# Kernel tuning notes

Measured on AMD Instinct MI355X. Metric: run time of the kernel, lower is better.

The kernel has to match this reference:

```python
import jax, jax.numpy as jnp
import numpy as np

N = 100000      # nodes
E = 3200000     # edges (avg degree 32)
F_IN = 128      # num_node_features
H = 16          # hidden dim (fixed in module)
C = 2           # num_classes


def setup_inputs() -> dict:
    key = jax.random.key(0)
    k0, k1, k2, k3 = jax.random.split(key, 4)
    x = jax.random.normal(k0, (N, F_IN), dtype=jnp.float32)
    edge_index = jax.random.randint(k1, (2, E), 0, N, dtype=jnp.int32)
    # GCNConv params: weight (in,out) + bias (out,) per layer (glorot-ish scale)
    W1 = jax.random.normal(k2, (F_IN, H), dtype=jnp.float32) * (1.0 / np.sqrt(F_IN))
    b1 = jnp.zeros((H,), jnp.float32)
    W2 = jax.random.normal(k3, (H, C), dtype=jnp.float32) * (1.0 / np.sqrt(H))
    b2 = jnp.zeros((C,), jnp.float32)
    return {"x": x, "edge_index": edge_index, "W1": W1, "b1": b1, "W2": W2, "b2": b2}


def _gcn_conv(x, W, b, src, dst, n):
    # GCNConv: h = D^{-1/2}(A+I)D^{-1/2} (x W) + b, with self-loops in src/dst
    h = x @ W                                   # [n, out]
    deg = jax.ops.segment_sum(jnp.ones_like(dst, dtype=h.dtype), dst, num_segments=n)
    dinv = jnp.where(deg > 0, jax.lax.rsqrt(deg), 0.0)
    norm = dinv[src] * dinv[dst]                # [E+n]
    msg = h[src] * norm[:, None]                # gather + scale
    out = jax.ops.segment_sum(msg, dst, num_segments=n)  # scatter-add
    return out + b


def reference(x, edge_index, W1, b1, W2, b2):
    loops = jnp.arange(N, dtype=edge_index.dtype)
    src = jnp.concatenate([edge_index[0], loops])
    dst = jnp.concatenate([edge_index[1], loops])
    h = jax.nn.relu(_gcn_conv(x, W1, b1, src, dst, N))
    # F.dropout(training=False) in eval mode is identity
    out = _gcn_conv(h, W2, b2, src, dst, N)
    return jax.nn.log_softmax(out, axis=1)
```

## Files before the change

kernel.cpp:

```cpp
#include <hip/hip_runtime.h>
#include <hip/hip_bf16.h>

#define NN 100000
#define NE 3200000
#define FIN 128
#define HD 16
#define CD 2

#define BSH 8
#define BSPAN 256
#define NBKT 391
#define CHUNK 8192
#define NPB ((NE + CHUNK - 1) / CHUNK)

__device__ __forceinline__ float bf2f(ushort u) {
    union { float f; unsigned int i; } v; v.i = ((unsigned int)u) << 16; return v.f;
}
__device__ __forceinline__ ushort f2b(float f) {
    union { float f; unsigned int u; } v; v.f = f;
    unsigned int r = (v.u + 0x7FFFu + ((v.u >> 16) & 1u)) >> 16;
    return (ushort)r;
}

__global__ __launch_bounds__(512) void k_cnt(const int* __restrict__ dst,
                                             int* __restrict__ cntmat) {
    __shared__ int h[NBKT];
    for (int i = threadIdx.x; i < NBKT; i += 512) h[i] = 0;
    __syncthreads();
    int cq = blockIdx.x * (CHUNK / 4);
    const int4* d4 = (const int4*)dst;
    #pragma unroll
    for (int j = 0; j < CHUNK / 2048; ++j) {
        int e4 = cq + j * 512 + threadIdx.x;
        if (e4 < NE / 4) {
            int4 d = d4[e4];
            atomicAdd(&h[d.x >> BSH], 1);
            atomicAdd(&h[d.y >> BSH], 1);
            atomicAdd(&h[d.z >> BSH], 1);
            atomicAdd(&h[d.w >> BSH], 1);
        }
    }
    __syncthreads();
    int* row = cntmat + (size_t)blockIdx.x * NBKT;
    for (int i = threadIdx.x; i < NBKT; i += 512) row[i] = h[i];
}

__global__ __launch_bounds__(256) void k_colscan(const int* __restrict__ cntmat,
                                                 int* __restrict__ relm,
                                                 int* __restrict__ btot) {
    __shared__ int sm[256];
    int j = blockIdx.x, t = threadIdx.x;
    int v[2];
    int b0 = t * 2;
    #pragma unroll
    for (int k = 0; k < 2; ++k) {
        int b = b0 + k;
        v[k] = (b < NPB) ? cntmat[(size_t)b * NBKT + j] : 0;
    }
    sm[t] = v[0] + v[1];
    __syncthreads();
    for (int off = 1; off < 256; off <<= 1) {
        int x = 0;
        if (t >= off) x = sm[t - off];
        __syncthreads();
        if (t >= off) sm[t] += x;
        __syncthreads();
    }
    int run = (t == 0) ? 0 : sm[t - 1];
    int* rrow = relm + (size_t)j * NPB;
    #pragma unroll
    for (int k = 0; k < 2; ++k) {
        int b = b0 + k;
        if (b < NPB) rrow[b] = run;
        run += v[k];
    }
    if (t == 255) btot[j] = sm[255];
}

__global__ __launch_bounds__(512) void k_scanb(const int* __restrict__ btot,
                                               int* __restrict__ boff) {
    __shared__ int sm[512];
    int t = threadIdx.x;
    sm[t] = (t < NBKT) ? btot[t] : 0;
    __syncthreads();
    for (int off = 1; off < 512; off <<= 1) {
        int v = 0;
        if (t >= off) v = sm[t - off];
        __syncthreads();
        if (t >= off) sm[t] += v;
        __syncthreads();
    }
    if (t < NBKT) boff[t] = t ? sm[t - 1] : 0;
    if (t == 511) boff[NBKT] = sm[511];
}

__global__ __launch_bounds__(512) void k_part(const int* __restrict__ src,
                                              const int* __restrict__ dst,
                                              const int* __restrict__ boff,
                                              const int* __restrict__ relm,
                                              unsigned int* __restrict__ csrb) {
    __shared__ int cur[NBKT];
    int b = blockIdx.x, t = threadIdx.x;
    for (int i = t; i < NBKT; i += 512)
        cur[i] = boff[i] + relm[(size_t)i * NPB + b];
    __syncthreads();
    int cq = b * (CHUNK / 4);
    const int4* s4 = (const int4*)src;
    const int4* d4 = (const int4*)dst;
    #pragma unroll
    for (int j = 0; j < CHUNK / 2048; ++j) {
        int e4 = cq + j * 512 + t;
        if (e4 < NE / 4) {
            int4 s = s4[e4];
            int4 d = d4[e4];
            int p;
            p = atomicAdd(&cur[d.x >> BSH], 1);
            csrb[p] = (unsigned)s.x | ((unsigned)(d.x & (BSPAN - 1)) << 17);
            p = atomicAdd(&cur[d.y >> BSH], 1);
            csrb[p] = (unsigned)s.y | ((unsigned)(d.y & (BSPAN - 1)) << 17);
            p = atomicAdd(&cur[d.z >> BSH], 1);
            csrb[p] = (unsigned)s.z | ((unsigned)(d.z & (BSPAN - 1)) << 17);
            p = atomicAdd(&cur[d.w >> BSH], 1);
            csrb[p] = (unsigned)s.w | ((unsigned)(d.w & (BSPAN - 1)) << 17);
        }
    }
}

__global__ __launch_bounds__(512) void k_sortb(const int* __restrict__ boff,
                                               const unsigned int* __restrict__ csrb,
                                               int* __restrict__ csr2,
                                               int* __restrict__ rowptr,
                                               float* __restrict__ dinv) {
    __shared__ int cnt[BSPAN];
    __shared__ int sc[BSPAN];
    __shared__ int cur[BSPAN];
    int b = blockIdx.x, t = threadIdx.x;
    if (t < BSPAN) cnt[t] = 0;
    __syncthreads();
    int e0 = boff[b], e1 = boff[b + 1];
    for (int e = e0 + t; e < e1; e += 512) atomicAdd(&cnt[csrb[e] >> 17], 1);
    __syncthreads();
    if (t < BSPAN) sc[t] = cnt[t];
    __syncthreads();
    for (int off = 1; off < BSPAN; off <<= 1) {
        int v = 0;
        if (t < BSPAN && t >= off) v = sc[t - off];
        __syncthreads();
        if (t < BSPAN && t >= off) sc[t] += v;
        __syncthreads();
    }
    if (t < BSPAN) {
        int ex = e0 + (t ? sc[t - 1] : 0);
        cur[t] = ex;
        int node = b * BSPAN + t;
        if (node < NN) {
            rowptr[node] = ex;
            dinv[node] = rsqrtf((float)cnt[t] + 1.0f);
        }
    }
    if (b == 0 && t == 0) rowptr[NN] = boff[NBKT];
    __syncthreads();
    for (int e = e0 + t; e < e1; e += 512) {
        unsigned p = csrb[e];
        int pos = atomicAdd(&cur[p >> 17], 1);
        csr2[pos] = (int)(p & 0x1FFFF);
    }
}

__global__ __launch_bounds__(256) void k_gemm1(const float* __restrict__ x,
                                               const float* __restrict__ W1,
                                               const float* __restrict__ dinv,
                                               ushort* __restrict__ h1b) {
    __shared__ float wsm[FIN][HD];
    for (int i = threadIdx.x; i < FIN * HD; i += 256) wsm[i >> 4][i & 15] = W1[i];
    __syncthreads();
    int t = blockIdx.x * 256 + threadIdx.x;
    int node = t >> 2;
    if (node >= NN) return;
    int g = (t & 3) * 4;
    const float4* xr = (const float4*)(x + (size_t)node * FIN);
    float a0 = 0.f, a1 = 0.f, a2 = 0.f, a3 = 0.f;
    #pragma unroll
    for (int k4 = 0; k4 < FIN / 4; ++k4) {
        float4 v = xr[k4];
        #pragma unroll
        for (int kk = 0; kk < 4; ++kk) {
            float vk = (kk == 0) ? v.x : (kk == 1) ? v.y : (kk == 2) ? v.z : v.w;
            float4 w = *(const float4*)&wsm[k4 * 4 + kk][g];
            a0 += vk * w.x;
            a1 += vk * w.y;
            a2 += vk * w.z;
            a3 += vk * w.w;
        }
    }
    float di = dinv[node];
    ushort4 r = {f2b(a0 * di), f2b(a1 * di), f2b(a2 * di), f2b(a3 * di)};
    *(ushort4*)(h1b + (size_t)node * HD + g) = r;
}

__global__ __launch_bounds__(256) void k_agg1(const int* __restrict__ rowptr,
                                              const int* __restrict__ csr2,
                                              const ushort* __restrict__ h1b,
                                              const float* __restrict__ dinv,
                                              const float* __restrict__ b1,
                                              const float* __restrict__ W2,
                                              float* __restrict__ g_s) {
    int wid = (blockIdx.x * 256 + threadIdx.x) >> 6;
    int lane = threadIdx.x & 63;
    int node = wid * 4 + (lane >> 4);
    if (node >= NN) return;
    int l16 = lane & 15;
    int slot = l16 >> 2;
    int fq = (lane & 3) * 4;
    int e0 = rowptr[node], e1 = rowptr[node + 1];
    float a0 = 0.f, a1 = 0.f, a2 = 0.f, a3 = 0.f;
    float c0 = 0.f, c1 = 0.f, c2 = 0.f, c3 = 0.f;
    int e = e0 + slot;
    for (; e + 4 < e1; e += 8) {
        int s0 = csr2[e];
        int s1 = csr2[e + 4];
        ushort4 u0 = *(const ushort4*)(h1b + (size_t)s0 * HD + fq);
        ushort4 u1 = *(const ushort4*)(h1b + (size_t)s1 * HD + fq);
        a0 += bf2f(u0.x); a1 += bf2f(u0.y); a2 += bf2f(u0.z); a3 += bf2f(u0.w);
        c0 += bf2f(u1.x); c1 += bf2f(u1.y); c2 += bf2f(u1.z); c3 += bf2f(u1.w);
    }
    if (e < e1) {
        ushort4 u = *(const ushort4*)(h1b + (size_t)csr2[e] * HD + fq);
        a0 += bf2f(u.x); a1 += bf2f(u.y); a2 += bf2f(u.z); a3 += bf2f(u.w);
    }
    a0 += c0; a1 += c1; a2 += c2; a3 += c3;
    #pragma unroll
    for (int m = 4; m <= 8; m <<= 1) {
        a0 += __shfl_xor(a0, m, 64);
        a1 += __shfl_xor(a1, m, 64);
        a2 += __shfl_xor(a2, m, 64);
        a3 += __shfl_xor(a3, m, 64);
    }
    if (slot == 0) {
        float di = dinv[node];
        ushort4 us = *(const ushort4*)(h1b + (size_t)node * HD + fq);
        float v0 = fmaxf(di * (a0 + bf2f(us.x)) + b1[fq],     0.f);
        float v1 = fmaxf(di * (a1 + bf2f(us.y)) + b1[fq + 1], 0.f);
        float v2 = fmaxf(di * (a2 + bf2f(us.z)) + b1[fq + 2], 0.f);
        float v3 = fmaxf(di * (a3 + bf2f(us.w)) + b1[fq + 3], 0.f);
        float p0 = v0 * W2[fq * 2]       + v1 * W2[(fq + 1) * 2]
                 + v2 * W2[(fq + 2) * 2] + v3 * W2[(fq + 3) * 2];
        float p1 = v0 * W2[fq * 2 + 1]       + v1 * W2[(fq + 1) * 2 + 1]
                 + v2 * W2[(fq + 2) * 2 + 1] + v3 * W2[(fq + 3) * 2 + 1];
        p0 += __shfl_xor(p0, 1, 64); p0 += __shfl_xor(p0, 2, 64);
        p1 += __shfl_xor(p1, 1, 64); p1 += __shfl_xor(p1, 2, 64);
        if (l16 == 0) {
            float2 r = {p0 * di, p1 * di};
            *(float2*)(g_s + (size_t)node * 2) = r;
        }
    }
}

__global__ __launch_bounds__(256) void k_agg2(const int* __restrict__ rowptr,
                                              const int* __restrict__ csr2,
                                              const float* __restrict__ g_s,
                                              const float* __restrict__ dinv,
                                              const float* __restrict__ b2,
                                              float* __restrict__ out) {
    int wid = (blockIdx.x * 256 + threadIdx.x) >> 6;
    int lane = threadIdx.x & 63;
    int node = wid * 4 + (lane >> 4);
    if (node >= NN) return;
    int l16 = lane & 15;
    int slot = l16 >> 1, f = lane & 1;
    int e0 = rowptr[node], e1 = rowptr[node + 1];
    float acc = 0.f;
    for (int e = e0 + slot; e < e1; e += 8)
        acc += g_s[(size_t)csr2[e] * 2 + f];
    #pragma unroll
    for (int m = 2; m <= 8; m <<= 1) acc += __shfl_xor(acc, m, 64);
    if (slot == 0) {
        float di = dinv[node];
        float o = di * (acc + g_s[(size_t)node * 2 + f]) + b2[f];
        float other = __shfl_xor(o, 1, 64);
        float mx = fmaxf(o, other);
        float l = mx + logf(__expf(o - mx) + __expf(other - mx));
        out[(size_t)node * 2 + f] = o - l;
    }
}

extern "C" void kernel_launch(void* const* d_in, const int* in_sizes, int n_in,
                              void* d_out, int out_size, void* d_ws, size_t ws_size,
                              hipStream_t stream) {
    const float* x   = (const float*)d_in[0];
    const int* ei    = (const int*)d_in[1];
    const int* src   = ei;
    const int* dst   = ei + NE;
    const float* W1  = (const float*)d_in[2];
    const float* b1  = (const float*)d_in[3];
    const float* W2  = (const float*)d_in[4];
    const float* b2  = (const float*)d_in[5];
    float* out = (float*)d_out;

    char* w = (char*)d_ws;
    float* dinv        = (float*)w;          w += NN * 4;
    int*   btot        = (int*)w;            w += NBKT * 4;
    int*   boff        = (int*)w;            w += (NBKT + 1) * 4;
    int*   rowptr      = (int*)w;            w += (NN + 1) * 4;
    int*   cntmat      = (int*)w;            w += (size_t)NPB * NBKT * 4;
    int*   relm        = (int*)w;            w += (size_t)NBKT * NPB * 4;
    unsigned int* csrb = (unsigned int*)w;   w += (size_t)NE * 4;
    int*   csr2        = (int*)w;            w += (size_t)NE * 4;
    ushort* h1b        = (ushort*)w;         w += (size_t)NN * HD * 2;
    float* g_s         = (float*)w;          w += NN * CD * 4;

    k_cnt    <<<NPB, 512, 0, stream>>>(dst, cntmat);
    k_colscan<<<NBKT, 256, 0, stream>>>(cntmat, relm, btot);
    k_scanb  <<<1, 512, 0, stream>>>(btot, boff);
    k_part   <<<NPB, 512, 0, stream>>>(src, dst, boff, relm, csrb);
    k_sortb  <<<NBKT, 512, 0, stream>>>(boff, csrb, csr2, rowptr, dinv);
    k_gemm1  <<<(NN * 4 + 255) / 256, 256, 0, stream>>>(x, W1, dinv, h1b);
    k_agg1   <<<(NN * 16 + 255) / 256, 256, 0, stream>>>(rowptr, csr2, h1b, dinv, b1, W2, g_s);
    k_agg2   <<<(NN * 16 + 255) / 256, 256, 0, stream>>>(rowptr, csr2, g_s, dinv, b2, out);
}
```

Before: 210.2 us.

## Fuse CSR build and first GEMM into one cooperative kernel with grid syncs

Replaces six separate kernels (count, column scan, bucket scan, partition, bucket sort, gemm1) with a single cooperative kernel that uses grid-wide syncs between phases, removing launch gaps. Bucket span is doubled to 512 so there are fewer buckets, which lets a single 512-thread block scan all partition counts per bucket. The grid is NPB blocks (391), which must all be co-resident for grid.sync. Phases that only use NBKT blocks leave about half the grid idle, and the GEMM phase becomes grid-stride.

Result: slower. 472.3 us (+124.6%).

```diff
diff --git a/kernel.cpp b/kernel.cpp
--- a/kernel.cpp
+++ b/kernel.cpp
@@ -1,5 +1,8 @@
 #include <hip/hip_runtime.h>
 #include <hip/hip_bf16.h>
+#include <hip/hip_cooperative_groups.h>
+
+namespace cg = cooperative_groups;
 
 #define NN 100000
 #define NE 3200000
@@ -7,9 +10,9 @@
 #define HD 16
 #define CD 2
 
-#define BSH 8
-#define BSPAN 256
-#define NBKT 391
+#define BSH 9
+#define BSPAN 512
+#define NBKT 196
 #define CHUNK 8192
 #define NPB ((NE + CHUNK - 1) / CHUNK)
 
@@ -22,180 +25,172 @@
     return (ushort)r;
 }
 
-__global__ __launch_bounds__(512) void k_cnt(const int* __restrict__ dst,
-                                             int* __restrict__ cntmat) {
-    __shared__ int h[NBKT];
-    for (int i = threadIdx.x; i < NBKT; i += 512) h[i] = 0;
-    __syncthreads();
-    int cq = blockIdx.x * (CHUNK / 4);
-    const int4* d4 = (const int4*)dst;
-    #pragma unroll
-    for (int j = 0; j < CHUNK / 2048; ++j) {
-        int e4 = cq + j * 512 + threadIdx.x;
-        if (e4 < NE / 4) {
-            int4 d = d4[e4];
-            atomicAdd(&h[d.x >> BSH], 1);
-            atomicAdd(&h[d.y >> BSH], 1);
-            atomicAdd(&h[d.z >> BSH], 1);
-            atomicAdd(&h[d.w >> BSH], 1);
-        }
-    }
-    __syncthreads();
-    int* row = cntmat + (size_t)blockIdx.x * NBKT;
-    for (int i = threadIdx.x; i < NBKT; i += 512) row[i] = h[i];
-}
-
-__global__ __launch_bounds__(256) void k_colscan(const int* __restrict__ cntmat,
-                                                 int* __restrict__ relm,
-                                                 int* __restrict__ btot) {
-    __shared__ int sm[256];
-    int j = blockIdx.x, t = threadIdx.x;
-    int v[2];
-    int b0 = t * 2;
-    #pragma unroll
-    for (int k = 0; k < 2; ++k) {
-        int b = b0 + k;
-        v[k] = (b < NPB) ? cntmat[(size_t)b * NBKT + j] : 0;
-    }
-    sm[t] = v[0] + v[1];
-    __syncthreads();
-    for (int off = 1; off < 256; off <<= 1) {
-        int x = 0;
-        if (t >= off) x = sm[t - off];
-        __syncthreads();
-        if (t >= off) sm[t] += x;
-        __syncthreads();
-    }
-    int run = (t == 0) ? 0 : sm[t - 1];
-    int* rrow = relm + (size_t)j * NPB;
-    #pragma unroll
-    for (int k = 0; k < 2; ++k) {
-        int b = b0 + k;
-        if (b < NPB) rrow[b] = run;
-        run += v[k];
-    }
-    if (t == 255) btot[j] = sm[255];
-}
-
-__global__ __launch_bounds__(512) void k_scanb(const int* __restrict__ btot,
-                                               int* __restrict__ boff) {
-    __shared__ int sm[512];
-    int t = threadIdx.x;
-    sm[t] = (t < NBKT) ? btot[t] : 0;
-    __syncthreads();
-    for (int off = 1; off < 512; off <<= 1) {
-        int v = 0;
-        if (t >= off) v = sm[t - off];
-        __syncthreads();
-        if (t >= off) sm[t] += v;
-        __syncthreads();
-    }
-    if (t < NBKT) boff[t] = t ? sm[t - 1] : 0;
-    if (t == 511) boff[NBKT] = sm[511];
-}
-
-__global__ __launch_bounds__(512) void k_part(const int* __restrict__ src,
+__global__ __launch_bounds__(512) void k_mega(const int* __restrict__ src,
                                               const int* __restrict__ dst,
-                                              const int* __restrict__ boff,
-                                              const int* __restrict__ relm,
-                                              unsigned int* __restrict__ csrb) {
-    __shared__ int cur[NBKT];
+                                              int* __restrict__ cntmat,
+                                              int* __restrict__ relm,
+                                              int* __restrict__ btot,
+                                              int* __restrict__ boff,
+                                              unsigned int* __restrict__ csrb,
+                                              int* __restrict__ csr2,
+                                              int* __restrict__ rowptr,
+                                              float* __restrict__ dinv,
+                                              const float* __restrict__ x,
+                                              const float* __restrict__ W1,
+                                              ushort* __restrict__ h1b) {
+    cg::grid_group grid = cg::this_grid();
+    __shared__ __align__(16) char smem[8192];
     int b = blockIdx.x, t = threadIdx.x;
-    for (int i = t; i < NBKT; i += 512)
-        cur[i] = boff[i] + relm[(size_t)i * NPB + b];
-    __syncthreads();
-    int cq = b * (CHUNK / 4);
-    const int4* s4 = (const int4*)src;
-    const int4* d4 = (const int4*)dst;
-    #pragma unroll
-    for (int j = 0; j < CHUNK / 2048; ++j) {
-        int e4 = cq + j * 512 + t;
-        if (e4 < NE / 4) {
-            int4 s = s4[e4];
-            int4 d = d4[e4];
-            int p;
-            p = atomicAdd(&cur[d.x >> BSH], 1);
-            csrb[p] = (unsigned)s.x | ((unsigned)(d.x & (BSPAN - 1)) << 17);
-            p = atomicAdd(&cur[d.y >> BSH], 1);
-            csrb[p] = (unsigned)s.y | ((unsigned)(d.y & (BSPAN - 1)) << 17);
-            p = atomicAdd(&cur[d.z >> BSH], 1);
-            csrb[p] = (unsigned)s.z | ((unsigned)(d.z & (BSPAN - 1)) << 17);
-            p = atomicAdd(&cur[d.w >> BSH], 1);
-            csrb[p] = (unsigned)s.w | ((unsigned)(d.w & (BSPAN - 1)) << 17);
-        }
-    }
-}
-
-__global__ __launch_bounds__(512) void k_sortb(const int* __restrict__ boff,
-                                               const unsigned int* __restrict__ csrb,
-                                               int* __restrict__ csr2,
-                                               int* __restrict__ rowptr,
-                                               float* __restrict__ dinv) {
-    __shared__ int cnt[BSPAN];
-    __shared__ int sc[BSPAN];
-    __shared__ int cur[BSPAN];
-    int b = blockIdx.x, t = threadIdx.x;
-    if (t < BSPAN) cnt[t] = 0;
-    __syncthreads();
-    int e0 = boff[b], e1 = boff[b + 1];
-    for (int e = e0 + t; e < e1; e += 512) atomicAdd(&cnt[csrb[e] >> 17], 1);
-    __syncthreads();
-    if (t < BSPAN) sc[t] = cnt[t];
-    __syncthreads();
-    for (int off = 1; off < BSPAN; off <<= 1) {
-        int v = 0;
-        if (t < BSPAN && t >= off) v = sc[t - off];
-        __syncthreads();
-        if (t < BSPAN && t >= off) sc[t] += v;
-        __syncthreads();
-    }
-    if (t < BSPAN) {
-        int ex = e0 + (t ? sc[t - 1] : 0);
-        cur[t] = ex;
-        int node = b * BSPAN + t;
-        if (node < NN) {
-            rowptr[node] = ex;
-            dinv[node] = rsqrtf((float)cnt[t] + 1.0f);
-        }
-    }
-    if (b == 0 && t == 0) rowptr[NN] = boff[NBKT];
-    __syncthreads();
-    for (int e = e0 + t; e < e1; e += 512) {
-        unsigned p = csrb[e];
-        int pos = atomicAdd(&cur[p >> 17], 1);
-        csr2[pos] = (int)(p & 0x1FFFF);
-    }
-}
-
-__global__ __launch_bounds__(256) void k_gemm1(const float* __restrict__ x,
-                                               const float* __restrict__ W1,
-                                               const float* __restrict__ dinv,
-                                               ushort* __restrict__ h1b) {
-    __shared__ float wsm[FIN][HD];
-    for (int i = threadIdx.x; i < FIN * HD; i += 256) wsm[i >> 4][i & 15] = W1[i];
-    __syncthreads();
-    int t = blockIdx.x * 256 + threadIdx.x;
-    int node = t >> 2;
-    if (node >= NN) return;
-    int g = (t & 3) * 4;
-    const float4* xr = (const float4*)(x + (size_t)node * FIN);
-    float a0 = 0.f, a1 = 0.f, a2 = 0.f, a3 = 0.f;
-    #pragma unroll
-    for (int k4 = 0; k4 < FIN / 4; ++k4) {
-        float4 v = xr[k4];
+
+    {
+        int* h = (int*)smem;
+        for (int i = t; i < NBKT; i += 512) h[i] = 0;
+        __syncthreads();
+        int cq = b * (CHUNK / 4);
+        const int4* d4 = (const int4*)dst;
         #pragma unroll
-        for (int kk = 0; kk < 4; ++kk) {
-            float vk = (kk == 0) ? v.x : (kk == 1) ? v.y : (kk == 2) ? v.z : v.w;
-            float4 w = *(const float4*)&wsm[k4 * 4 + kk][g];
-            a0 += vk * w.x;
-            a1 += vk * w.y;
-            a2 += vk * w.z;
-            a3 += vk * w.w;
-        }
-    }
-    float di = dinv[node];
-    ushort4 r = {f2b(a0 * di), f2b(a1 * di), f2b(a2 * di), f2b(a3 * di)};
-    *(ushort4*)(h1b + (size_t)node * HD + g) = r;
+        for (int j = 0; j < CHUNK / 2048; ++j) {
+            int e4 = cq + j * 512 + t;
+            if (e4 < NE / 4) {
+                int4 d = d4[e4];
+                atomicAdd(&h[d.x >> BSH], 1);
+                atomicAdd(&h[d.y >> BSH], 1);
+                atomicAdd(&h[d.z >> BSH], 1);
+                atomicAdd(&h[d.w >> BSH], 1);
+            }
+        }
+        __syncthreads();
+        int* row = cntmat + (size_t)b * NBKT;
+        for (int i = t; i < NBKT; i += 512) row[i] = h[i];
+    }
+    grid.sync();
+
+    if (b < NBKT) {
+        int* sm = (int*)smem;
+        int v = (t < NPB) ? cntmat[(size_t)t * NBKT + b] : 0;
+        sm[t] = v;
+        __syncthreads();
+        for (int off = 1; off < 512; off <<= 1) {
+            int u = 0;
+            if (t >= off) u = sm[t - off];
+            __syncthreads();
+            if (t >= off) sm[t] += u;
+            __syncthreads();
+        }
+        if (t < NPB) relm[(size_t)b * NPB + t] = t ? sm[t - 1] : 0;
+        if (t == 511) btot[b] = sm[511];
+    }
+    grid.sync();
+
+    if (b == 0) {
+        int* sm = (int*)smem;
+        sm[t] = (t < NBKT) ? btot[t] : 0;
+        __syncthreads();
+        for (int off = 1; off < 512; off <<= 1) {
+            int v = 0;
+            if (t >= off) v = sm[t - off];
+            __syncthreads();
+            if (t >= off) sm[t] += v;
+            __syncthreads();
+        }
+        if (t < NBKT) boff[t] = t ? sm[t - 1] : 0;
+        if (t == 511) boff[NBKT] = sm[511];
+    }
+    grid.sync();
+
+    {
+        int* cur = (int*)smem;
+        for (int i = t; i < NBKT; i += 512)
+            cur[i] = boff[i] + relm[(size_t)i * NPB + b];
+        __syncthreads();
+        int cq = b * (CHUNK / 4);
+        const int4* s4 = (const int4*)src;
+        const int4* d4 = (const int4*)dst;
+        #pragma unroll
+        for (int j = 0; j < CHUNK / 2048; ++j) {
+            int e4 = cq + j * 512 + t;
+            if (e4 < NE / 4) {
+                int4 s = s4[e4];
+                int4 d = d4[e4];
+                int p;
+                p = atomicAdd(&cur[d.x >> BSH], 1);
+                csrb[p] = (unsigned)s.x | ((unsigned)(d.x & (BSPAN - 1)) << 17);
+                p = atomicAdd(&cur[d.y >> BSH], 1);
+                csrb[p] = (unsigned)s.y | ((unsigned)(d.y & (BSPAN - 1)) << 17);
+                p = atomicAdd(&cur[d.z >> BSH], 1);
+                csrb[p] = (unsigned)s.z | ((unsigned)(d.z & (BSPAN - 1)) << 17);
+                p = atomicAdd(&cur[d.w >> BSH], 1);
+                csrb[p] = (unsigned)s.w | ((unsigned)(d.w & (BSPAN - 1)) << 17);
+            }
+        }
+    }
+    grid.sync();
+
+    if (b < NBKT) {
+        int* scnt = (int*)smem;
+        int* ssc  = scnt + BSPAN;
+        int* scur = ssc + BSPAN;
+        if (t < BSPAN) scnt[t] = 0;
+        __syncthreads();
+        int e0 = boff[b], e1 = boff[b + 1];
+        for (int e = e0 + t; e < e1; e += 512) atomicAdd(&scnt[csrb[e] >> 17], 1);
+        __syncthreads();
+        ssc[t] = scnt[t];
+        __syncthreads();
+        for (int off = 1; off < BSPAN; off <<= 1) {
+            int v = 0;
+            if (t >= off) v = ssc[t - off];
+            __syncthreads();
+            if (t >= off) ssc[t] += v;
+            __syncthreads();
+        }
+        {
+            int ex = e0 + (t ? ssc[t - 1] : 0);
+            scur[t] = ex;
+            int node = b * BSPAN + t;
+            if (node < NN) {
+                rowptr[node] = ex;
+                dinv[node] = rsqrtf((float)scnt[t] + 1.0f);
+            }
+        }
+        if (b == 0 && t == 0) rowptr[NN] = boff[NBKT];
+        __syncthreads();
+        for (int e = e0 + t; e < e1; e += 512) {
+            unsigned p = csrb[e];
+            int pos = atomicAdd(&scur[p >> 17], 1);
+            csr2[pos] = (int)(p & 0x1FFFF);
+        }
+    }
+    grid.sync();
+
+    {
+        float (*wsm)[HD] = (float(*)[HD])smem;
+        __syncthreads();
+        for (int i = t; i < FIN * HD; i += 512) wsm[i >> 4][i & 15] = W1[i];
+        __syncthreads();
+        for (int task = b * 512 + t; task < NN * 4; task += gridDim.x * 512) {
+            int node = task >> 2;
+            int g = (task & 3) * 4;
+            const float4* xr = (const float4*)(x + (size_t)node * FIN);
+            float a0 = 0.f, a1 = 0.f, a2 = 0.f, a3 = 0.f;
+            #pragma unroll
+            for (int k4 = 0; k4 < FIN / 4; ++k4) {
+                float4 v = xr[k4];
+                #pragma unroll
+                for (int kk = 0; kk < 4; ++kk) {
+                    float vk = (kk == 0) ? v.x : (kk == 1) ? v.y : (kk == 2) ? v.z : v.w;
+                    float4 w = *(const float4*)&wsm[k4 * 4 + kk][g];
+                    a0 += vk * w.x;
+                    a1 += vk * w.y;
+                    a2 += vk * w.z;
+                    a3 += vk * w.w;
+                }
+            }
+            float di = dinv[node];
+            ushort4 r = {f2b(a0 * di), f2b(a1 * di), f2b(a2 * di), f2b(a3 * di)};
+            *(ushort4*)(h1b + (size_t)node * HD + g) = r;
+        }
+    }
 }
 
 __global__ __launch_bounds__(256) void k_agg1(const int* __restrict__ rowptr,
@@ -309,12 +304,11 @@
     ushort* h1b        = (ushort*)w;         w += (size_t)NN * HD * 2;
     float* g_s         = (float*)w;          w += NN * CD * 4;
 
-    k_cnt    <<<NPB, 512, 0, stream>>>(dst, cntmat);
-    k_colscan<<<NBKT, 256, 0, stream>>>(cntmat, relm, btot);
-    k_scanb  <<<1, 512, 0, stream>>>(btot, boff);
-    k_part   <<<NPB, 512, 0, stream>>>(src, dst, boff, relm, csrb);
-    k_sortb  <<<NBKT, 512, 0, stream>>>(boff, csrb, csr2, rowptr, dinv);
-    k_gemm1  <<<(NN * 4 + 255) / 256, 256, 0, stream>>>(x, W1, dinv, h1b);
-    k_agg1   <<<(NN * 16 + 255) / 256, 256, 0, stream>>>(rowptr, csr2, h1b, dinv, b1, W2, g_s);
-    k_agg2   <<<(NN * 16 + 255) / 256, 256, 0, stream>>>(rowptr, csr2, g_s, dinv, b2, out);
-}
+    void* margs[] = { (void*)&src, (void*)&dst, (void*)&cntmat, (void*)&relm,
+                      (void*)&btot, (void*)&boff, (void*)&csrb, (void*)&csr2,
+                      (void*)&rowptr, (void*)&dinv, (void*)&x, (void*)&W1,
+                      (void*)&h1b };
+    hipLaunchCooperativeKernel((void*)k_mega, dim3(NPB), dim3(512), margs, 0, stream);
+    k_agg1<<<(NN * 16 + 255) / 256, 256, 0, stream>>>(rowptr, csr2, h1b, dinv, b1, W2, g_s);
+    k_agg2<<<(NN * 16 + 255) / 256, 256, 0, stream>>>(rowptr, csr2, g_s, dinv, b2, out);
+}
```

## Drop per-node CSR sort; aggregate bucketed edges with LDS atomics

Applied to the files above, without the earlier changes.

Removes the per-bucket counting sort that built rowptr/csr2. Aggregation now works directly on the bucket-partitioned edge list, with each 256-node bucket block accumulating into shared memory via atomics. The degree count and the first GEMM are fused into one kernel per bucket. This saves a pass over the edges and the csr2 write. In exchange it adds LDS atomic contention and runs only 391 large blocks, which may leave the GPU's compute units underused.

Measured after the change: 532.0 us. +153.0%, slower.

```diff
diff --git a/kernel.cpp b/kernel.cpp
--- a/kernel.cpp
+++ b/kernel.cpp
@@ -126,161 +126,127 @@
     }
 }
 
-__global__ __launch_bounds__(512) void k_sortb(const int* __restrict__ boff,
-                                               const unsigned int* __restrict__ csrb,
-                                               int* __restrict__ csr2,
-                                               int* __restrict__ rowptr,
-                                               float* __restrict__ dinv) {
+__global__ __launch_bounds__(512) void k_dg(const int* __restrict__ boff,
+                                            const unsigned int* __restrict__ csrb,
+                                            const float* __restrict__ x,
+                                            const float* __restrict__ W1,
+                                            float* __restrict__ dinv,
+                                            ushort* __restrict__ h1b) {
+    __shared__ float wsm[FIN][HD];
     __shared__ int cnt[BSPAN];
-    __shared__ int sc[BSPAN];
-    __shared__ int cur[BSPAN];
-    int b = blockIdx.x, t = threadIdx.x;
+    __shared__ float sdv[BSPAN];
+    int b = blockIdx.x, t = threadIdx.x;
+    for (int i = t; i < FIN * HD; i += 512) wsm[i >> 4][i & 15] = W1[i];
     if (t < BSPAN) cnt[t] = 0;
     __syncthreads();
     int e0 = boff[b], e1 = boff[b + 1];
     for (int e = e0 + t; e < e1; e += 512) atomicAdd(&cnt[csrb[e] >> 17], 1);
     __syncthreads();
-    if (t < BSPAN) sc[t] = cnt[t];
-    __syncthreads();
-    for (int off = 1; off < BSPAN; off <<= 1) {
-        int v = 0;
-        if (t < BSPAN && t >= off) v = sc[t - off];
-        __syncthreads();
-        if (t < BSPAN && t >= off) sc[t] += v;
-        __syncthreads();
-    }
     if (t < BSPAN) {
-        int ex = e0 + (t ? sc[t - 1] : 0);
-        cur[t] = ex;
+        float di = rsqrtf((float)cnt[t] + 1.0f);
+        sdv[t] = di;
         int node = b * BSPAN + t;
-        if (node < NN) {
-            rowptr[node] = ex;
-            dinv[node] = rsqrtf((float)cnt[t] + 1.0f);
-        }
-    }
-    if (b == 0 && t == 0) rowptr[NN] = boff[NBKT];
-    __syncthreads();
-    for (int e = e0 + t; e < e1; e += 512) {
-        unsigned p = csrb[e];
-        int pos = atomicAdd(&cur[p >> 17], 1);
-        csr2[pos] = (int)(p & 0x1FFFF);
-    }
-}
-
-__global__ __launch_bounds__(256) void k_gemm1(const float* __restrict__ x,
-                                               const float* __restrict__ W1,
-                                               const float* __restrict__ dinv,
-                                               ushort* __restrict__ h1b) {
-    __shared__ float wsm[FIN][HD];
-    for (int i = threadIdx.x; i < FIN * HD; i += 256) wsm[i >> 4][i & 15] = W1[i];
-    __syncthreads();
-    int t = blockIdx.x * 256 + threadIdx.x;
-    int node = t >> 2;
-    if (node >= NN) return;
-    int g = (t & 3) * 4;
-    const float4* xr = (const float4*)(x + (size_t)node * FIN);
-    float a0 = 0.f, a1 = 0.f, a2 = 0.f, a3 = 0.f;
-    #pragma unroll
-    for (int k4 = 0; k4 < FIN / 4; ++k4) {
-        float4 v = xr[k4];
+        if (node < NN) dinv[node] = di;
+    }
+    __syncthreads();
+    #pragma unroll
+    for (int it = 0; it < 2; ++it) {
+        int task = it * 512 + t;
+        int nl = task >> 2;
+        int node = b * BSPAN + nl;
+        if (node >= NN) break;
+        int g = (task & 3) * 4;
+        const float4* xr = (const float4*)(x + (size_t)node * FIN);
+        float a0 = 0.f, a1 = 0.f, a2 = 0.f, a3 = 0.f;
         #pragma unroll
-        for (int kk = 0; kk < 4; ++kk) {
-            float vk = (kk == 0) ? v.x : (kk == 1) ? v.y : (kk == 2) ? v.z : v.w;
-            float4 w = *(const float4*)&wsm[k4 * 4 + kk][g];
-            a0 += vk * w.x;
-            a1 += vk * w.y;
-            a2 += vk * w.z;
-            a3 += vk * w.w;
-        }
-    }
-    float di = dinv[node];
-    ushort4 r = {f2b(a0 * di), f2b(a1 * di), f2b(a2 * di), f2b(a3 * di)};
-    *(ushort4*)(h1b + (size_t)node * HD + g) = r;
-}
-
-__global__ __launch_bounds__(256) void k_agg1(const int* __restrict__ rowptr,
-                                              const int* __restrict__ csr2,
+        for (int k4 = 0; k4 < FIN / 4; ++k4) {
+            float4 v = xr[k4];
+            #pragma unroll
+            for (int kk = 0; kk < 4; ++kk) {
+                float vk = (kk == 0) ? v.x : (kk == 1) ? v.y : (kk == 2) ? v.z : v.w;
+                float4 w = *(const float4*)&wsm[k4 * 4 + kk][g];
+                a0 += vk * w.x;
+                a1 += vk * w.y;
+                a2 += vk * w.z;
+                a3 += vk * w.w;
+            }
+        }
+        float di = sdv[nl];
+        ushort4 r = {f2b(a0 * di), f2b(a1 * di), f2b(a2 * di), f2b(a3 * di)};
+        *(ushort4*)(h1b + (size_t)node * HD + g) = r;
+    }
+}
+
+__global__ __launch_bounds__(512) void k_agg1(const int* __restrict__ boff,
+                                              const unsigned int* __restrict__ csrb,
                                               const ushort* __restrict__ h1b,
                                               const float* __restrict__ dinv,
                                               const float* __restrict__ b1,
                                               const float* __restrict__ W2,
                                               float* __restrict__ g_s) {
-    int wid = (blockIdx.x * 256 + threadIdx.x) >> 6;
-    int lane = threadIdx.x & 63;
-    int node = wid * 4 + (lane >> 4);
-    if (node >= NN) return;
-    int l16 = lane & 15;
-    int slot = l16 >> 2;
-    int fq = (lane & 3) * 4;
-    int e0 = rowptr[node], e1 = rowptr[node + 1];
-    float a0 = 0.f, a1 = 0.f, a2 = 0.f, a3 = 0.f;
-    float c0 = 0.f, c1 = 0.f, c2 = 0.f, c3 = 0.f;
-    int e = e0 + slot;
-    for (; e + 4 < e1; e += 8) {
-        int s0 = csr2[e];
-        int s1 = csr2[e + 4];
-        ushort4 u0 = *(const ushort4*)(h1b + (size_t)s0 * HD + fq);
-        ushort4 u1 = *(const ushort4*)(h1b + (size_t)s1 * HD + fq);
-        a0 += bf2f(u0.x); a1 += bf2f(u0.y); a2 += bf2f(u0.z); a3 += bf2f(u0.w);
-        c0 += bf2f(u1.x); c1 += bf2f(u1.y); c2 += bf2f(u1.z); c3 += bf2f(u1.w);
-    }
-    if (e < e1) {
-        ushort4 u = *(const ushort4*)(h1b + (size_t)csr2[e] * HD + fq);
-        a0 += bf2f(u.x); a1 += bf2f(u.y); a2 += bf2f(u.z); a3 += bf2f(u.w);
-    }
-    a0 += c0; a1 += c1; a2 += c2; a3 += c3;
-    #pragma unroll
-    for (int m = 4; m <= 8; m <<= 1) {
-        a0 += __shfl_xor(a0, m, 64);
-        a1 += __shfl_xor(a1, m, 64);
-        a2 += __shfl_xor(a2, m, 64);
-        a3 += __shfl_xor(a3, m, 64);
-    }
-    if (slot == 0) {
+    __shared__ float acc[BSPAN * 17];
+    int b = blockIdx.x, t = threadIdx.x;
+    for (int i = t; i < BSPAN * 17; i += 512) acc[i] = 0.f;
+    __syncthreads();
+    int grp = t >> 4, f = t & 15;
+    int e0 = boff[b], e1 = boff[b + 1];
+    int e = e0 + grp;
+    for (; e + 32 < e1; e += 64) {
+        unsigned p0 = csrb[e];
+        unsigned p1 = csrb[e + 32];
+        float v0 = bf2f(h1b[(size_t)(p0 & 0x1FFFF) * HD + f]);
+        float v1 = bf2f(h1b[(size_t)(p1 & 0x1FFFF) * HD + f]);
+        atomicAdd(&acc[(p0 >> 17) * 17 + f], v0);
+        atomicAdd(&acc[(p1 >> 17) * 17 + f], v1);
+    }
+    for (; e < e1; e += 32) {
+        unsigned p = csrb[e];
+        atomicAdd(&acc[(p >> 17) * 17 + f], bf2f(h1b[(size_t)(p & 0x1FFFF) * HD + f]));
+    }
+    __syncthreads();
+    int node = b * BSPAN + t;
+    if (t < BSPAN && node < NN) {
         float di = dinv[node];
-        ushort4 us = *(const ushort4*)(h1b + (size_t)node * HD + fq);
-        float v0 = fmaxf(di * (a0 + bf2f(us.x)) + b1[fq],     0.f);
-        float v1 = fmaxf(di * (a1 + bf2f(us.y)) + b1[fq + 1], 0.f);
-        float v2 = fmaxf(di * (a2 + bf2f(us.z)) + b1[fq + 2], 0.f);
-        float v3 = fmaxf(di * (a3 + bf2f(us.w)) + b1[fq + 3], 0.f);
-        float p0 = v0 * W2[fq * 2]       + v1 * W2[(fq + 1) * 2]
-                 + v2 * W2[(fq + 2) * 2] + v3 * W2[(fq + 3) * 2];
-        float p1 = v0 * W2[fq * 2 + 1]       + v1 * W2[(fq + 1) * 2 + 1]
-                 + v2 * W2[(fq + 2) * 2 + 1] + v3 * W2[(fq + 3) * 2 + 1];
-        p0 += __shfl_xor(p0, 1, 64); p0 += __shfl_xor(p0, 2, 64);
-        p1 += __shfl_xor(p1, 1, 64); p1 += __shfl_xor(p1, 2, 64);
-        if (l16 == 0) {
-            float2 r = {p0 * di, p1 * di};
-            *(float2*)(g_s + (size_t)node * 2) = r;
-        }
-    }
-}
-
-__global__ __launch_bounds__(256) void k_agg2(const int* __restrict__ rowptr,
-                                              const int* __restrict__ csr2,
+        float p0 = 0.f, p1 = 0.f;
+        #pragma unroll
+        for (int k = 0; k < HD; ++k) {
+            float v = fmaxf(di * (acc[t * 17 + k] + bf2f(h1b[(size_t)node * HD + k])) + b1[k], 0.f);
+            p0 += v * W2[k * 2];
+            p1 += v * W2[k * 2 + 1];
+        }
+        float2 r = {p0 * di, p1 * di};
+        *(float2*)(g_s + (size_t)node * 2) = r;
+    }
+}
+
+__global__ __launch_bounds__(512) void k_agg2(const int* __restrict__ boff,
+                                              const unsigned int* __restrict__ csrb,
                                               const float* __restrict__ g_s,
                                               const float* __restrict__ dinv,
                                               const float* __restrict__ b2,
                                               float* __restrict__ out) {
-    int wid = (blockIdx.x * 256 + threadIdx.x) >> 6;
-    int lane = threadIdx.x & 63;
-    int node = wid * 4 + (lane >> 4);
-    if (node >= NN) return;
-    int l16 = lane & 15;
-    int slot = l16 >> 1, f = lane & 1;
-    int e0 = rowptr[node], e1 = rowptr[node + 1];
-    float acc = 0.f;
-    for (int e = e0 + slot; e < e1; e += 8)
-        acc += g_s[(size_t)csr2[e] * 2 + f];
-    #pragma unroll
-    for (int m = 2; m <= 8; m <<= 1) acc += __shfl_xor(acc, m, 64);
-    if (slot == 0) {
+    __shared__ float acc[BSPAN * 3];
+    int b = blockIdx.x, t = threadIdx.x;
+    for (int i = t; i < BSPAN * 3; i += 512) acc[i] = 0.f;
+    __syncthreads();
+    int e0 = boff[b], e1 = boff[b + 1];
+    for (int e = e0 + t; e < e1; e += 512) {
+        unsigned p = csrb[e];
+        float2 gv = *(const float2*)(g_s + (size_t)(p & 0x1FFFF) * 2);
+        int dl = p >> 17;
+        atomicAdd(&acc[dl * 3],     gv.x);
+        atomicAdd(&acc[dl * 3 + 1], gv.y);
+    }
+    __syncthreads();
+    int node = b * BSPAN + t;
+    if (t < BSPAN && node < NN) {
         float di = dinv[node];
-        float o = di * (acc + g_s[(size_t)node * 2 + f]) + b2[f];
-        float other = __shfl_xor(o, 1, 64);
-        float mx = fmaxf(o, other);
-        float l = mx + logf(__expf(o - mx) + __expf(other - mx));
-        out[(size_t)node * 2 + f] = o - l;
+        float o0 = di * (acc[t * 3]     + g_s[(size_t)node * 2])     + b2[0];
+        float o1 = di * (acc[t * 3 + 1] + g_s[(size_t)node * 2 + 1]) + b2[1];
+        float mx = fmaxf(o0, o1);
+        float l = mx + logf(__expf(o0 - mx) + __expf(o1 - mx));
+        out[(size_t)node * 2]     = o0 - l;
+        out[(size_t)node * 2 + 1] = o1 - l;
     }
 }
 
@@ -301,11 +267,9 @@
     float* dinv        = (float*)w;          w += NN * 4;
     int*   btot        = (int*)w;            w += NBKT * 4;
     int*   boff        = (int*)w;            w += (NBKT + 1) * 4;
-    int*   rowptr      = (int*)w;            w += (NN + 1) * 4;
     int*   cntmat      = (int*)w;            w += (size_t)NPB * NBKT * 4;
     int*   relm        = (int*)w;            w += (size_t)NBKT * NPB * 4;
     unsigned int* csrb = (unsigned int*)w;   w += (size_t)NE * 4;
-    int*   csr2        = (int*)w;            w += (size_t)NE * 4;
     ushort* h1b        = (ushort*)w;         w += (size_t)NN * HD * 2;
     float* g_s         = (float*)w;          w += NN * CD * 4;
 
@@ -313,8 +277,7 @@
     k_colscan<<<NBKT, 256, 0, stream>>>(cntmat, relm, btot);
     k_scanb  <<<1, 512, 0, stream>>>(btot, boff);
     k_part   <<<NPB, 512, 0, stream>>>(src, dst, boff, relm, csrb);
-    k_sortb  <<<NBKT, 512, 0, stream>>>(boff, csrb, csr2, rowptr, dinv);
-    k_gemm1  <<<(NN * 4 + 255) / 256, 256, 0, stream>>>(x, W1, dinv, h1b);
-    k_agg1   <<<(NN * 16 + 255) / 256, 256, 0, stream>>>(rowptr, csr2, h1b, dinv, b1, W2, g_s);
-    k_agg2   <<<(NN * 16 + 255) / 256, 256, 0, stream>>>(rowptr, csr2, g_s, dinv, b2, out);
-}
+    k_dg     <<<NBKT, 512, 0, stream>>>(boff, csrb, x, W1, dinv, h1b);
+    k_agg1   <<<NBKT, 512, 0, stream>>>(boff, csrb, h1b, dinv, b1, W2, g_s);
+    k_agg2   <<<NBKT, 512, 0, stream>>>(boff, csrb, g_s, dinv, b2, out);
+}
```

## Fuse layer-1 GEMM into bucket sort kernel and widen buckets to 512 nodes

Applied to the files above, without the earlier changes.

Bucket width doubles to 512 nodes, which halves the bucket count and lets the column scan use one element per thread. The per-bucket counting sort is merged with the x·W1 projection, so each bucket block computes h1 for its own nodes using the degree-normalisation held in shared memory. This removes one kernel launch and the global dinv reread. The cost is that the bandwidth-heavy read of x now runs on only ~196 blocks after the sort phase, which may reduce memory parallelism.

Result: slower. 219.1 us (+4.2%).

```diff
diff --git a/kernel.cpp b/kernel.cpp
--- a/kernel.cpp
+++ b/kernel.cpp
@@ -7,9 +7,9 @@
 #define HD 16
 #define CD 2
 
-#define BSH 8
-#define BSPAN 256
-#define NBKT 391
+#define BSH 9
+#define BSPAN 512
+#define NBKT 196
 #define CHUNK 8192
 #define NPB ((NE + CHUNK - 1) / CHUNK)
 
@@ -45,45 +45,32 @@
     for (int i = threadIdx.x; i < NBKT; i += 512) row[i] = h[i];
 }
 
-__global__ __launch_bounds__(256) void k_colscan(const int* __restrict__ cntmat,
+__global__ __launch_bounds__(512) void k_colscan(const int* __restrict__ cntmat,
                                                  int* __restrict__ relm,
                                                  int* __restrict__ btot) {
+    __shared__ int sm[512];
+    int j = blockIdx.x, t = threadIdx.x;
+    int v = (t < NPB) ? cntmat[(size_t)t * NBKT + j] : 0;
+    sm[t] = v;
+    __syncthreads();
+    for (int off = 1; off < 512; off <<= 1) {
+        int u = 0;
+        if (t >= off) u = sm[t - off];
+        __syncthreads();
+        if (t >= off) sm[t] += u;
+        __syncthreads();
+    }
+    if (t < NPB) relm[(size_t)j * NPB + t] = t ? sm[t - 1] : 0;
+    if (t == 511) btot[j] = sm[511];
+}
+
+__global__ __launch_bounds__(256) void k_scanb(const int* __restrict__ btot,
+                                               int* __restrict__ boff) {
     __shared__ int sm[256];
-    int j = blockIdx.x, t = threadIdx.x;
-    int v[2];
-    int b0 = t * 2;
-    #pragma unroll
-    for (int k = 0; k < 2; ++k) {
-        int b = b0 + k;
-        v[k] = (b < NPB) ? cntmat[(size_t)b * NBKT + j] : 0;
-    }
-    sm[t] = v[0] + v[1];
-    __syncthreads();
-    for (int off = 1; off < 256; off <<= 1) {
-        int x = 0;
-        if (t >= off) x = sm[t - off];
-        __syncthreads();
-        if (t >= off) sm[t] += x;
-        __syncthreads();
-    }
-    int run = (t == 0) ? 0 : sm[t - 1];
-    int* rrow = relm + (size_t)j * NPB;
-    #pragma unroll
-    for (int k = 0; k < 2; ++k) {
-        int b = b0 + k;
-        if (b < NPB) rrow[b] = run;
-        run += v[k];
-    }
-    if (t == 255) btot[j] = sm[255];
-}
-
-__global__ __launch_bounds__(512) void k_scanb(const int* __restrict__ btot,
-                                               int* __restrict__ boff) {
-    __shared__ int sm[512];
     int t = threadIdx.x;
     sm[t] = (t < NBKT) ? btot[t] : 0;
     __syncthreads();
-    for (int off = 1; off < 512; off <<= 1) {
+    for (int off = 1; off < 256; off <<= 1) {
         int v = 0;
         if (t >= off) v = sm[t - off];
         __syncthreads();
@@ -91,7 +78,7 @@
         __syncthreads();
     }
     if (t < NBKT) boff[t] = t ? sm[t - 1] : 0;
-    if (t == 511) boff[NBKT] = sm[511];
+    if (t == 255) boff[NBKT] = sm[255];
 }
 
 __global__ __launch_bounds__(512) void k_part(const int* __restrict__ src,
@@ -126,36 +113,44 @@
     }
 }
 
-__global__ __launch_bounds__(512) void k_sortb(const int* __restrict__ boff,
-                                               const unsigned int* __restrict__ csrb,
-                                               int* __restrict__ csr2,
-                                               int* __restrict__ rowptr,
-                                               float* __restrict__ dinv) {
+__global__ __launch_bounds__(512) void k_dg(const int* __restrict__ boff,
+                                            const unsigned int* __restrict__ csrb,
+                                            const float* __restrict__ x,
+                                            const float* __restrict__ W1,
+                                            int* __restrict__ csr2,
+                                            int* __restrict__ rowptr,
+                                            float* __restrict__ dinv,
+                                            ushort* __restrict__ h1b) {
+    __shared__ float wsm[FIN][HD];
     __shared__ int cnt[BSPAN];
     __shared__ int sc[BSPAN];
     __shared__ int cur[BSPAN];
+    __shared__ float sdv[BSPAN];
     int b = blockIdx.x, t = threadIdx.x;
-    if (t < BSPAN) cnt[t] = 0;
+    for (int i = t; i < FIN * HD; i += 512) wsm[i >> 4][i & 15] = W1[i];
+    cnt[t] = 0;
     __syncthreads();
     int e0 = boff[b], e1 = boff[b + 1];
     for (int e = e0 + t; e < e1; e += 512) atomicAdd(&cnt[csrb[e] >> 17], 1);
     __syncthreads();
-    if (t < BSPAN) sc[t] = cnt[t];
+    sc[t] = cnt[t];
     __syncthreads();
     for (int off = 1; off < BSPAN; off <<= 1) {
         int v = 0;
-        if (t < BSPAN && t >= off) v = sc[t - off];
-        __syncthreads();
-        if (t < BSPAN && t >= off) sc[t] += v;
-        __syncthreads();
-    }
-    if (t < BSPAN) {
+        if (t >= off) v = sc[t - off];
+        __syncthreads();
+        if (t >= off) sc[t] += v;
+        __syncthreads();
+    }
+    {
         int ex = e0 + (t ? sc[t - 1] : 0);
         cur[t] = ex;
+        float di = rsqrtf((float)cnt[t] + 1.0f);
+        sdv[t] = di;
         int node = b * BSPAN + t;
         if (node < NN) {
             rowptr[node] = ex;
-            dinv[node] = rsqrtf((float)cnt[t] + 1.0f);
+            dinv[node] = di;
         }
     }
     if (b == 0 && t == 0) rowptr[NN] = boff[NBKT];
@@ -165,37 +160,32 @@
         int pos = atomicAdd(&cur[p >> 17], 1);
         csr2[pos] = (int)(p & 0x1FFFF);
     }
-}
-
-__global__ __launch_bounds__(256) void k_gemm1(const float* __restrict__ x,
-                                               const float* __restrict__ W1,
-                                               const float* __restrict__ dinv,
-                                               ushort* __restrict__ h1b) {
-    __shared__ float wsm[FIN][HD];
-    for (int i = threadIdx.x; i < FIN * HD; i += 256) wsm[i >> 4][i & 15] = W1[i];
-    __syncthreads();
-    int t = blockIdx.x * 256 + threadIdx.x;
-    int node = t >> 2;
-    if (node >= NN) return;
-    int g = (t & 3) * 4;
-    const float4* xr = (const float4*)(x + (size_t)node * FIN);
-    float a0 = 0.f, a1 = 0.f, a2 = 0.f, a3 = 0.f;
-    #pragma unroll
-    for (int k4 = 0; k4 < FIN / 4; ++k4) {
-        float4 v = xr[k4];
+    #pragma unroll
+    for (int it = 0; it < 4; ++it) {
+        int task = it * 512 + t;
+        int nl = task >> 2;
+        int node = b * BSPAN + nl;
+        if (node >= NN) break;
+        int g = (task & 3) * 4;
+        const float4* xr = (const float4*)(x + (size_t)node * FIN);
+        float a0 = 0.f, a1 = 0.f, a2 = 0.f, a3 = 0.f;
         #pragma unroll
-        for (int kk = 0; kk < 4; ++kk) {
-            float vk = (kk == 0) ? v.x : (kk == 1) ? v.y : (kk == 2) ? v.z : v.w;
-            float4 w = *(const float4*)&wsm[k4 * 4 + kk][g];
-            a0 += vk * w.x;
-            a1 += vk * w.y;
-            a2 += vk * w.z;
-            a3 += vk * w.w;
-        }
-    }
-    float di = dinv[node];
-    ushort4 r = {f2b(a0 * di), f2b(a1 * di), f2b(a2 * di), f2b(a3 * di)};
-    *(ushort4*)(h1b + (size_t)node * HD + g) = r;
+        for (int k4 = 0; k4 < FIN / 4; ++k4) {
+            float4 v = xr[k4];
+            #pragma unroll
+            for (int kk = 0; kk < 4; ++kk) {
+                float vk = (kk == 0) ? v.x : (kk == 1) ? v.y : (kk == 2) ? v.z : v.w;
+                float4 w = *(const float4*)&wsm[k4 * 4 + kk][g];
+                a0 += vk * w.x;
+                a1 += vk * w.y;
+                a2 += vk * w.z;
+                a3 += vk * w.w;
+            }
+        }
+        float di = sdv[nl];
+        ushort4 r = {f2b(a0 * di), f2b(a1 * di), f2b(a2 * di), f2b(a3 * di)};
+        *(ushort4*)(h1b + (size_t)node * HD + g) = r;
+    }
 }
 
 __global__ __launch_bounds__(256) void k_agg1(const int* __restrict__ rowptr,
@@ -310,11 +300,10 @@
     float* g_s         = (float*)w;          w += NN * CD * 4;
 
     k_cnt    <<<NPB, 512, 0, stream>>>(dst, cntmat);
-    k_colscan<<<NBKT, 256, 0, stream>>>(cntmat, relm, btot);
-    k_scanb  <<<1, 512, 0, stream>>>(btot, boff);
+    k_colscan<<<NBKT, 512, 0, stream>>>(cntmat, relm, btot);
+    k_scanb  <<<1, 256, 0, stream>>>(btot, boff);
     k_part   <<<NPB, 512, 0, stream>>>(src, dst, boff, relm, csrb);
-    k_sortb  <<<NBKT, 512, 0, stream>>>(boff, csrb, csr2, rowptr, dinv);
-    k_gemm1  <<<(NN * 4 + 255) / 256, 256, 0, stream>>>(x, W1, dinv, h1b);
+    k_dg     <<<NBKT, 512, 0, stream>>>(boff, csrb, x, W1, csr2, rowptr, dinv, h1b);
     k_agg1   <<<(NN * 16 + 255) / 256, 256, 0, stream>>>(rowptr, csr2, h1b, dinv, b1, W2, g_s);
     k_agg2   <<<(NN * 16 + 255) / 256, 256, 0, stream>>>(rowptr, csr2, g_s, dinv, b2, out);
 }
```
